# Performance work log

Hardware: AMD Instinct MI355X
Metric: run time of the kernel (lower is better)

## Reference

```python
import jax, jax.numpy as jnp
import numpy as np

N = 16777216  # number of sample points
L = 2         # n_layers


def _layer_unitary(w):
    """U = RZ(w2) @ RY(w1) @ RX(w0), each a standard 2x2 rotation gate."""
    h = w * 0.5
    c, s = jnp.cos(h), jnp.sin(h)
    i = jnp.complex64(1j)
    rx = jnp.array([[1, 0], [0, 1]], jnp.complex64) * c[0] + jnp.array([[0, 1], [1, 0]], jnp.complex64) * (-i * s[0])
    ry = jnp.array([[c[1], -s[1]], [s[1], c[1]]], jnp.complex64)
    rz = jnp.array([[jnp.exp(-i * h[2]), 0.0 + 0.0j], [0.0 + 0.0j, jnp.exp(i * h[2])]], jnp.complex64)
    return rz @ ry @ rx


def setup_inputs() -> dict:
    key = jax.random.key(0)
    k1, k2 = jax.random.split(key)
    x = jax.random.normal(k1, (N, 1), dtype=jnp.float32)
    weights = 0.1 * jax.random.normal(k2, (L, 3), dtype=jnp.float32)
    a = jnp.asarray(1.0, jnp.float32)
    b = jnp.asarray(0.0, jnp.float32)
    return {"x": x, "weights": weights, "a": a, "b": b}


def reference(x, weights, a, b):
    # Total weight-only unitary: product over layers (applied layer 0 first).
    U = jnp.eye(2, dtype=jnp.complex64)
    for l in range(weights.shape[0]):  # static, tiny (L=2)
        U = _layer_unitary(weights[l]) @ U
    # RY(x)|0> = [cos(x/2), sin(x/2)]
    xh = 0.5 * x.reshape(-1)
    state0 = jnp.stack([jnp.cos(xh), jnp.sin(xh)], axis=-1).astype(jnp.complex64)  # [N,2]
    s = jnp.einsum('ij,nj->ni', U, state0)  # [N,2]
    z = (s[:, 0].real ** 2 + s[:, 0].imag ** 2) - (s[:, 1].real ** 2 + s[:, 1].imag ** 2)
    return a * z.reshape(-1, 1) + b
```

## Files before the change

kernel.cpp:

```cpp
#include <hip/hip_runtime.h>


struct cplx { float re, im; };

__device__ inline cplx cmul(cplx p, cplx q) {
    cplx r;
    r.re = p.re * q.re - p.im * q.im;
    r.im = p.re * q.im + p.im * q.re;
    return r;
}
__device__ inline cplx cadd(cplx p, cplx q) { return cplx{p.re + q.re, p.im + q.im}; }

__global__ __launch_bounds__(256) void qpinn_kernel(
    const float* __restrict__ x, const float* __restrict__ w,
    const float* __restrict__ pa, const float* __restrict__ pb,
    float* __restrict__ out, int n4) {

    const float a = pa[0];
    const float b = pb[0];

    cplx U00{1.f, 0.f}, U01{0.f, 0.f}, U10{0.f, 0.f}, U11{1.f, 0.f};

    #pragma unroll
    for (int l = 0; l < 2; ++l) {
        const float h0 = 0.5f * w[3 * l + 0];
        const float h1 = 0.5f * w[3 * l + 1];
        const float h2 = 0.5f * w[3 * l + 2];
        float c0, s0, c1, s1, c2, s2;
        __sincosf(h0, &s0, &c0);
        __sincosf(h1, &s1, &c1);
        __sincosf(h2, &s2, &c2);

        cplx X00{c0, 0.f}, X01{0.f, -s0}, X10{0.f, -s0}, X11{c0, 0.f};
        cplx Y00{c1, 0.f}, Y01{-s1, 0.f}, Y10{s1, 0.f}, Y11{c1, 0.f};
        cplx A00 = cadd(cmul(Y00, X00), cmul(Y01, X10));
        cplx A01 = cadd(cmul(Y00, X01), cmul(Y01, X11));
        cplx A10 = cadd(cmul(Y10, X00), cmul(Y11, X10));
        cplx A11 = cadd(cmul(Y10, X01), cmul(Y11, X11));
        cplx zm{c2, -s2}, zp{c2, s2};
        cplx L00 = cmul(zm, A00), L01 = cmul(zm, A01);
        cplx L10 = cmul(zp, A10), L11 = cmul(zp, A11);
        cplx n00 = cadd(cmul(L00, U00), cmul(L01, U10));
        cplx n01 = cadd(cmul(L00, U01), cmul(L01, U11));
        cplx n10 = cadd(cmul(L10, U00), cmul(L11, U10));
        cplx n11 = cadd(cmul(L10, U01), cmul(L11, U11));
        U00 = n00; U01 = n01; U10 = n10; U11 = n11;
    }

    const float A = (U00.re * U00.re + U00.im * U00.im) - (U10.re * U10.re + U10.im * U10.im);
    const float B = (U01.re * U01.re + U01.im * U01.im) - (U11.re * U11.re + U11.im * U11.im);
    const float C = 2.f * ((U00.re * U01.re + U00.im * U01.im) -
                           (U10.re * U11.re + U10.im * U11.im));

    const float K0 = fmaf(a, 0.5f * (A + B), b);
    const float K1 = a * 0.5f * (A - B);
    const float K2 = a * 0.5f * C;

    const float4* __restrict__ x4 = (const float4*)x;
    float4* __restrict__ o4 = (float4*)out;

    const int stride = gridDim.x * blockDim.x;
    for (int i = blockIdx.x * blockDim.x + threadIdx.x; i < n4; i += stride) {
        float4 v = x4[i];
        float4 r;
        float sx, cx;
        __sincosf(v.x, &sx, &cx); r.x = fmaf(K1, cx, fmaf(K2, sx, K0));
        __sincosf(v.y, &sx, &cx); r.y = fmaf(K1, cx, fmaf(K2, sx, K0));
        __sincosf(v.z, &sx, &cx); r.z = fmaf(K1, cx, fmaf(K2, sx, K0));
        __sincosf(v.w, &sx, &cx); r.w = fmaf(K1, cx, fmaf(K2, sx, K0));
        o4[i] = r;
    }
}

extern "C" void kernel_launch(void* const* d_in, const int* in_sizes, int n_in,
                              void* d_out, int out_size, void* d_ws, size_t ws_size,
                              hipStream_t stream) {
    const float* x = (const float*)d_in[0];
    const float* w = (const float*)d_in[1];
    const float* a = (const float*)d_in[2];
    const float* b = (const float*)d_in[3];
    float* out = (float*)d_out;

    const int n = in_sizes[0];
    const int n4 = n / 4;
    const int block = 256;
    const int grid = (n4 + block * 2 - 1) / (block * 2);

    qpinn_kernel<<<grid, block, 0, stream>>>(x, w, a, b, out, n4);
}
```

Measured before the change: 115.7 us.

## Fold sin/cos pair into single phase-shifted hardware cosine and precompute coefficients

Rewrites the per-element K1*cos+K2*sin as R*cos(x - phi), evaluated with the hardware v_cos instruction on a revolutions-scaled argument, so each element needs one transcendental instead of a sincos pair. The coefficient setup (unitary product, atan2, sqrt) moves to a single-thread kernel writing to workspace when one is available; otherwise a fused kernel computes it per thread as before. The grid is fixed at 2048 blocks of 256 threads in a grid-stride loop. This adds a second kernel launch and relies on the accuracy of the hardware cosine for large arguments.

```diff
diff --git a/kernel.cpp b/kernel.cpp
--- a/kernel.cpp
+++ b/kernel.cpp
@@ -4,32 +4,22 @@
 struct cplx { float re, im; };
 
 __device__ inline cplx cmul(cplx p, cplx q) {
-    cplx r;
-    r.re = p.re * q.re - p.im * q.im;
-    r.im = p.re * q.im + p.im * q.re;
-    return r;
+    return cplx{p.re * q.re - p.im * q.im, p.re * q.im + p.im * q.re};
 }
 __device__ inline cplx cadd(cplx p, cplx q) { return cplx{p.re + q.re, p.im + q.im}; }
 
-__global__ __launch_bounds__(256) void qpinn_kernel(
-    const float* __restrict__ x, const float* __restrict__ w,
-    const float* __restrict__ pa, const float* __restrict__ pb,
-    float* __restrict__ out, int n4) {
-
-    const float a = pa[0];
-    const float b = pb[0];
-
+__device__ inline void qpinn_coeffs(const float* __restrict__ w, float a, float b,
+                                    float& K0, float& R, float& mphirev) {
     cplx U00{1.f, 0.f}, U01{0.f, 0.f}, U10{0.f, 0.f}, U11{1.f, 0.f};
-
     #pragma unroll
     for (int l = 0; l < 2; ++l) {
         const float h0 = 0.5f * w[3 * l + 0];
         const float h1 = 0.5f * w[3 * l + 1];
         const float h2 = 0.5f * w[3 * l + 2];
         float c0, s0, c1, s1, c2, s2;
-        __sincosf(h0, &s0, &c0);
-        __sincosf(h1, &s1, &c1);
-        __sincosf(h2, &s2, &c2);
+        sincosf(h0, &s0, &c0);
+        sincosf(h1, &s1, &c1);
+        sincosf(h2, &s2, &c2);
 
         cplx X00{c0, 0.f}, X01{0.f, -s0}, X10{0.f, -s0}, X11{c0, 0.f};
         cplx Y00{c1, 0.f}, Y01{-s1, 0.f}, Y10{s1, 0.f}, Y11{c1, 0.f};
@@ -46,15 +36,35 @@
         cplx n11 = cadd(cmul(L10, U01), cmul(L11, U11));
         U00 = n00; U01 = n01; U10 = n10; U11 = n11;
     }
-
     const float A = (U00.re * U00.re + U00.im * U00.im) - (U10.re * U10.re + U10.im * U10.im);
     const float B = (U01.re * U01.re + U01.im * U01.im) - (U11.re * U11.re + U11.im * U11.im);
     const float C = 2.f * ((U00.re * U01.re + U00.im * U01.im) -
                            (U10.re * U11.re + U10.im * U11.im));
-
-    const float K0 = fmaf(a, 0.5f * (A + B), b);
+    K0 = fmaf(a, 0.5f * (A + B), b);
     const float K1 = a * 0.5f * (A - B);
     const float K2 = a * 0.5f * C;
+    R = sqrtf(K1 * K1 + K2 * K2);
+    const float INV2PI = 0.15915494309189535f;
+    mphirev = -atan2f(K2, K1) * INV2PI;
+}
+
+__global__ void coeff_kernel(const float* __restrict__ w, const float* __restrict__ pa,
+                             const float* __restrict__ pb, float* __restrict__ coef) {
+    if (threadIdx.x == 0) {
+        float K0, R, mphirev;
+        qpinn_coeffs(w, pa[0], pb[0], K0, R, mphirev);
+        coef[0] = K0; coef[1] = R; coef[2] = mphirev;
+    }
+}
+
+__global__ __launch_bounds__(256) void stream_kernel(
+    const float* __restrict__ x, const float* __restrict__ coef,
+    float* __restrict__ out, int n4) {
+
+    const float K0 = coef[0];
+    const float R  = coef[1];
+    const float mphirev = coef[2];
+    const float INV2PI = 0.15915494309189535f;
 
     const float4* __restrict__ x4 = (const float4*)x;
     float4* __restrict__ o4 = (float4*)out;
@@ -63,11 +73,34 @@
     for (int i = blockIdx.x * blockDim.x + threadIdx.x; i < n4; i += stride) {
         float4 v = x4[i];
         float4 r;
-        float sx, cx;
-        __sincosf(v.x, &sx, &cx); r.x = fmaf(K1, cx, fmaf(K2, sx, K0));
-        __sincosf(v.y, &sx, &cx); r.y = fmaf(K1, cx, fmaf(K2, sx, K0));
-        __sincosf(v.z, &sx, &cx); r.z = fmaf(K1, cx, fmaf(K2, sx, K0));
-        __sincosf(v.w, &sx, &cx); r.w = fmaf(K1, cx, fmaf(K2, sx, K0));
+        r.x = fmaf(R, __builtin_amdgcn_cosf(fmaf(v.x, INV2PI, mphirev)), K0);
+        r.y = fmaf(R, __builtin_amdgcn_cosf(fmaf(v.y, INV2PI, mphirev)), K0);
+        r.z = fmaf(R, __builtin_amdgcn_cosf(fmaf(v.z, INV2PI, mphirev)), K0);
+        r.w = fmaf(R, __builtin_amdgcn_cosf(fmaf(v.w, INV2PI, mphirev)), K0);
+        o4[i] = r;
+    }
+}
+
+__global__ __launch_bounds__(256) void fused_kernel(
+    const float* __restrict__ x, const float* __restrict__ w,
+    const float* __restrict__ pa, const float* __restrict__ pb,
+    float* __restrict__ out, int n4) {
+
+    float K0, R, mphirev;
+    qpinn_coeffs(w, pa[0], pb[0], K0, R, mphirev);
+    const float INV2PI = 0.15915494309189535f;
+
+    const float4* __restrict__ x4 = (const float4*)x;
+    float4* __restrict__ o4 = (float4*)out;
+
+    const int stride = gridDim.x * blockDim.x;
+    for (int i = blockIdx.x * blockDim.x + threadIdx.x; i < n4; i += stride) {
+        float4 v = x4[i];
+        float4 r;
+        r.x = fmaf(R, __builtin_amdgcn_cosf(fmaf(v.x, INV2PI, mphirev)), K0);
+        r.y = fmaf(R, __builtin_amdgcn_cosf(fmaf(v.y, INV2PI, mphirev)), K0);
+        r.z = fmaf(R, __builtin_amdgcn_cosf(fmaf(v.z, INV2PI, mphirev)), K0);
+        r.w = fmaf(R, __builtin_amdgcn_cosf(fmaf(v.w, INV2PI, mphirev)), K0);
         o4[i] = r;
     }
 }
@@ -84,7 +117,13 @@
     const int n = in_sizes[0];
     const int n4 = n / 4;
     const int block = 256;
-    const int grid = (n4 + block * 2 - 1) / (block * 2);
+    const int grid = 2048;
 
-    qpinn_kernel<<<grid, block, 0, stream>>>(x, w, a, b, out, n4);
+    if (d_ws != nullptr && ws_size >= 16) {
+        float* coef = (float*)d_ws;
+        coeff_kernel<<<1, 64, 0, stream>>>(w, a, b, coef);
+        stream_kernel<<<grid, block, 0, stream>>>(x, coef, out, n4);
+    } else {
+        fused_kernel<<<grid, block, 0, stream>>>(x, w, a, b, out, n4);
+    }
 }
```

Result: slower. 120.2 us (+3.9%).
